# Kernel optimization log

Hardware: AMD Instinct MI355X
Metric: run time of the kernel (lower is better)

Reference implementation:

```python
import jax, jax.numpy as jnp
import numpy as np

R, C = 4096, 4096  # weight matrix rows (output channels) x cols


def setup_inputs() -> dict:
    key = jax.random.key(0)
    k1, k2, k3 = jax.random.split(key, 3)
    x = jax.random.normal(k1, (R, C), jnp.float32) * 0.1  # weight-like values
    # per-output-channel positive/negative scales (|xmax|/(maxq/2), |xmin|/(maxq/2))
    scale_pos = jax.random.uniform(k2, (R, 1), jnp.float32, minval=0.02, maxval=0.2)
    scale_neg = jax.random.uniform(k3, (R, 1), jnp.float32, minval=0.02, maxval=0.2)
    # fixed AF4 4-bit codebook from Quantizer_af4.configure (bits==4)
    code = jnp.array([-6., -4., -3., -2., -1.5, -1., -0.5, -0.,
                      0., 0.5, 1., 1.5, 2., 3., 4., 6.], jnp.float32)
    tensor_max = jnp.array([0.4], jnp.float32)
    tensor_min = jnp.array([-0.4], jnp.float32)
    return dict(x=x, scale_pos=scale_pos, scale_neg=scale_neg, code=code,
                tensor_max=tensor_max, tensor_min=tensor_min)


def _nearest_code(q, code):
    # argmin over the 16-entry codebook, then gather the chosen code value
    idx = jnp.argmin(jnp.abs(q[..., None] - code), axis=-1)  # [R, C]
    return jnp.take(code, idx)                               # [R, C]


def reference(x, scale_pos, scale_neg, code, tensor_max, tensor_min):
    x = jnp.clip(x, tensor_min, tensor_max)
    x_pos = jnp.where(x >= 0, x, 0.0)
    x_neg = jnp.where(x < 0, x, 0.0)
    q_pos = _nearest_code(x_pos / scale_pos, code)
    q_neg = _nearest_code(x_neg / scale_neg, code)
    return q_pos * scale_pos + q_neg * scale_neg
```

## Files before the change

kernel.cpp:

```cpp
#include <hip/hip_runtime.h>


__global__ __launch_bounds__(256) void af4_v11_rd_fast(
    const float* __restrict__ xin,
    const float* __restrict__ s_pos,
    const float* __restrict__ s_neg,
    const float* __restrict__ t_max,
    const float* __restrict__ t_min,
    float* __restrict__ yout)
{
    const double BP0 = 0.25 + 0x1p-25, BP1 = 0.75 + 0x1p-24,
                 BP2 = 1.25 + 0x1p-23, BP3 = 1.75 + 0x1p-23,
                 BP4 = 2.50 + 0x1p-22, BP5 = 3.50 + 0x1p-22,
                 BP6 = 5.00 + 0x1p-21;
    const double BN0 = 0.25 - 0x1p-26, BN1 = 0.75 - 0x1p-24,
                 BN2 = 1.25 - 0x1p-23, BN3 = 1.75 - 0x1p-23,
                 BN4 = 2.50 - 0x1p-22, BN5 = 3.50 - 0x1p-22,
                 BN6 = 5.00 - 0x1p-21;

    const int row = blockIdx.x >> 2;
    const float sp = s_pos[row];
    const float sn = s_neg[row];
    const float hi = t_max[0];
    const float lo = t_min[0];

    const double dsp = (double)sp, dsn = (double)sn;
    const double tp0 = BP0*dsp, tp1 = BP1*dsp, tp2 = BP2*dsp, tp3 = BP3*dsp,
                 tp4 = BP4*dsp, tp5 = BP5*dsp, tp6 = BP6*dsp;
    const double tn0 = BN0*dsn, tn1 = BN1*dsn, tn2 = BN2*dsn, tn3 = BN3*dsn,
                 tn4 = BN4*dsn, tn5 = BN5*dsn, tn6 = BN6*dsn;

    const size_t base = (size_t)blockIdx.x * 1024;
    const float4 v = ((const float4*)(xin + base))[threadIdx.x];
    float r[4] = {v.x, v.y, v.z, v.w};
    float o[4];

    #pragma unroll
    for (int k = 0; k < 4; ++k) {
        const float xv = fminf(fmaxf(r[k], lo), hi);
        const bool pos = (xv >= 0.0f);
        const double a = (double)fabsf(xv);

        if (pos) {
            float m = 0.0f;
            m += (a >= tp0) ? 0.5f : 0.0f;
            m += (a >= tp1) ? 0.5f : 0.0f;
            m += (a >= tp2) ? 0.5f : 0.0f;
            m += (a >= tp3) ? 0.5f : 0.0f;
            m += (a >= tp4) ? 1.0f : 0.0f;
            m += (a >= tp5) ? 1.0f : 0.0f;
            m += (a >= tp6) ? 2.0f : 0.0f;
            o[k] = m * sp;
        } else {
            float m = 0.0f;
            m += (a > tn0) ? 0.5f : 0.0f;
            m += (a > tn1) ? 0.5f : 0.0f;
            m += (a > tn2) ? 0.5f : 0.0f;
            m += (a > tn3) ? 0.5f : 0.0f;
            m += (a > tn4) ? 1.0f : 0.0f;
            m += (a > tn5) ? 1.0f : 0.0f;
            m += (a > tn6) ? 2.0f : 0.0f;
            o[k] = (-m) * sn;
        }
    }

    float4 w; w.x = o[0]; w.y = o[1]; w.z = o[2]; w.w = o[3];
    ((float4*)(yout + base))[threadIdx.x] = w;
}

extern "C" void kernel_launch(void* const* d_in, const int* in_sizes, int n_in,
                              void* d_out, int out_size, void* d_ws, size_t ws_size,
                              hipStream_t stream) {
    const float* x    = (const float*)d_in[0];
    const float* sp   = (const float*)d_in[1];
    const float* sn   = (const float*)d_in[2];
    const float* tmax = (const float*)d_in[4];
    const float* tmin = (const float*)d_in[5];
    float* out = (float*)d_out;

    const int rows = in_sizes[1];
    dim3 grid(rows * 4), block(256);
    af4_v11_rd_fast<<<grid, block, 0, stream>>>(x, sp, sn, tmax, tmin, out);
}
```

Before: 118.7 us.

## Replace per-element double compares with exact float32 per-row thresholds

Precomputes each row's quantization thresholds once in double and rounds them to exactly equivalent float32 values (ceiling or successor), so per-element comparisons run in fp32 instead of fp64. Each block now handles a whole row with four float4 loads per thread issued up front, and results are written with nontemporal stores. This removes the costly fp64 conversion and compare work from the inner loop. It relies on the rounding helpers preserving the exact tie behaviour, and it reduces the grid size while adding more work per thread.

```diff
diff --git a/kernel.cpp b/kernel.cpp
--- a/kernel.cpp
+++ b/kernel.cpp
@@ -1,7 +1,37 @@
 #include <hip/hip_runtime.h>
 
 
-__global__ __launch_bounds__(256) void af4_v11_rd_fast(
+typedef float vfloat4 __attribute__((ext_vector_type(4)));
+
+__device__ __forceinline__ float f32_ceil_ge(double t) {
+    float c = (float)t;
+    if ((double)c < t) c = __uint_as_float(__float_as_uint(c) + 1u);
+    return c;
+}
+__device__ __forceinline__ float f32_succ_gt(double t) {
+    float c = (float)t;
+    if ((double)c <= t) c = __uint_as_float(__float_as_uint(c) + 1u);
+    return c;
+}
+
+__device__ __forceinline__ float af4_elem(float xv, float sp, float nsn,
+                                          float lo, float hi,
+                                          const float* __restrict__ cp,
+                                          const float* __restrict__ cn) {
+    xv = fminf(fmaxf(xv, lo), hi);
+    const bool pos = (xv >= 0.0f);
+    const float a = fabsf(xv);
+    const float st[7] = {0.5f, 0.5f, 0.5f, 0.5f, 1.0f, 1.0f, 2.0f};
+    float m = 0.0f;
+    #pragma unroll
+    for (int i = 0; i < 7; ++i) {
+        const float t = pos ? cp[i] : cn[i];
+        m += (a >= t) ? st[i] : 0.0f;
+    }
+    return m * (pos ? sp : nsn);
+}
+
+__global__ __launch_bounds__(256) void af4_v13_f32thr(
     const float* __restrict__ xin,
     const float* __restrict__ s_pos,
     const float* __restrict__ s_neg,
@@ -9,63 +39,47 @@
     const float* __restrict__ t_min,
     float* __restrict__ yout)
 {
-    const double BP0 = 0.25 + 0x1p-25, BP1 = 0.75 + 0x1p-24,
-                 BP2 = 1.25 + 0x1p-23, BP3 = 1.75 + 0x1p-23,
-                 BP4 = 2.50 + 0x1p-22, BP5 = 3.50 + 0x1p-22,
-                 BP6 = 5.00 + 0x1p-21;
-    const double BN0 = 0.25 - 0x1p-26, BN1 = 0.75 - 0x1p-24,
-                 BN2 = 1.25 - 0x1p-23, BN3 = 1.75 - 0x1p-23,
-                 BN4 = 2.50 - 0x1p-22, BN5 = 3.50 - 0x1p-22,
-                 BN6 = 5.00 - 0x1p-21;
-
-    const int row = blockIdx.x >> 2;
+    const int row = blockIdx.x;
     const float sp = s_pos[row];
     const float sn = s_neg[row];
     const float hi = t_max[0];
     const float lo = t_min[0];
 
     const double dsp = (double)sp, dsn = (double)sn;
-    const double tp0 = BP0*dsp, tp1 = BP1*dsp, tp2 = BP2*dsp, tp3 = BP3*dsp,
-                 tp4 = BP4*dsp, tp5 = BP5*dsp, tp6 = BP6*dsp;
-    const double tn0 = BN0*dsn, tn1 = BN1*dsn, tn2 = BN2*dsn, tn3 = BN3*dsn,
-                 tn4 = BN4*dsn, tn5 = BN5*dsn, tn6 = BN6*dsn;
+    float cp[7], cn[7];
+    cp[0] = f32_ceil_ge((0.25 + 0x1p-25) * dsp);
+    cp[1] = f32_ceil_ge((0.75 + 0x1p-24) * dsp);
+    cp[2] = f32_ceil_ge((1.25 + 0x1p-23) * dsp);
+    cp[3] = f32_ceil_ge((1.75 + 0x1p-23) * dsp);
+    cp[4] = f32_ceil_ge((2.50 + 0x1p-22) * dsp);
+    cp[5] = f32_ceil_ge((3.50 + 0x1p-22) * dsp);
+    cp[6] = f32_ceil_ge((5.00 + 0x1p-21) * dsp);
+    cn[0] = f32_succ_gt((0.25 - 0x1p-26) * dsn);
+    cn[1] = f32_succ_gt((0.75 - 0x1p-24) * dsn);
+    cn[2] = f32_succ_gt((1.25 - 0x1p-23) * dsn);
+    cn[3] = f32_succ_gt((1.75 - 0x1p-23) * dsn);
+    cn[4] = f32_succ_gt((2.50 - 0x1p-22) * dsn);
+    cn[5] = f32_succ_gt((3.50 - 0x1p-22) * dsn);
+    cn[6] = f32_succ_gt((5.00 - 0x1p-21) * dsn);
+    const float nsn = -sn;
 
-    const size_t base = (size_t)blockIdx.x * 1024;
-    const float4 v = ((const float4*)(xin + base))[threadIdx.x];
-    float r[4] = {v.x, v.y, v.z, v.w};
-    float o[4];
+    const size_t base = (size_t)row * 4096;
+    const vfloat4* __restrict__ src = (const vfloat4*)(xin + base);
+    vfloat4* __restrict__ dst = (vfloat4*)(yout + base);
+
+    vfloat4 v[4];
+    #pragma unroll
+    for (int j = 0; j < 4; ++j) v[j] = src[threadIdx.x + 256 * j];
 
     #pragma unroll
-    for (int k = 0; k < 4; ++k) {
-        const float xv = fminf(fmaxf(r[k], lo), hi);
-        const bool pos = (xv >= 0.0f);
-        const double a = (double)fabsf(xv);
-
-        if (pos) {
-            float m = 0.0f;
-            m += (a >= tp0) ? 0.5f : 0.0f;
-            m += (a >= tp1) ? 0.5f : 0.0f;
-            m += (a >= tp2) ? 0.5f : 0.0f;
-            m += (a >= tp3) ? 0.5f : 0.0f;
-            m += (a >= tp4) ? 1.0f : 0.0f;
-            m += (a >= tp5) ? 1.0f : 0.0f;
-            m += (a >= tp6) ? 2.0f : 0.0f;
-            o[k] = m * sp;
-        } else {
-            float m = 0.0f;
-            m += (a > tn0) ? 0.5f : 0.0f;
-            m += (a > tn1) ? 0.5f : 0.0f;
-            m += (a > tn2) ? 0.5f : 0.0f;
-            m += (a > tn3) ? 0.5f : 0.0f;
-            m += (a > tn4) ? 1.0f : 0.0f;
-            m += (a > tn5) ? 1.0f : 0.0f;
-            m += (a > tn6) ? 2.0f : 0.0f;
-            o[k] = (-m) * sn;
-        }
+    for (int j = 0; j < 4; ++j) {
+        vfloat4 o;
+        o.x = af4_elem(v[j].x, sp, nsn, lo, hi, cp, cn);
+        o.y = af4_elem(v[j].y, sp, nsn, lo, hi, cp, cn);
+        o.z = af4_elem(v[j].z, sp, nsn, lo, hi, cp, cn);
+        o.w = af4_elem(v[j].w, sp, nsn, lo, hi, cp, cn);
+        __builtin_nontemporal_store(o, &dst[threadIdx.x + 256 * j]);
     }
-
-    float4 w; w.x = o[0]; w.y = o[1]; w.z = o[2]; w.w = o[3];
-    ((float4*)(yout + base))[threadIdx.x] = w;
 }
 
 extern "C" void kernel_launch(void* const* d_in, const int* in_sizes, int n_in,
@@ -79,6 +93,6 @@
     float* out = (float*)d_out;
 
     const int rows = in_sizes[1];
-    dim3 grid(rows * 4), block(256);
-    af4_v11_rd_fast<<<grid, block, 0, stream>>>(x, sp, sn, tmax, tmin, out);
+    dim3 grid(rows), block(256);
+    af4_v13_f32thr<<<grid, block, 0, stream>>>(x, sp, sn, tmax, tmin, out);
 }
```

Measured after the change: 114.8 us. 1.03x faster.
